# Performance work log

Measured on AMD Instinct MI355X. Metric: run time of the kernel, lower is better.

Reference implementation:

```python
import jax, jax.numpy as jnp
import numpy as np
from math import sqrt

KEY_DIM = 128
N_NODES = 1_000_000
N_GRAPHS = 8192


def setup_inputs() -> dict:
    key = jax.random.key(0)
    k1, k2, k3 = jax.random.split(key, 3)
    V = jax.random.normal(k1, (N_NODES, KEY_DIM), dtype=jnp.float32)
    Q = jax.random.normal(k2, (N_GRAPHS, KEY_DIM), dtype=jnp.float32)
    batch_node_index = jnp.sort(
        jax.random.randint(k3, (N_NODES,), 0, N_GRAPHS, dtype=jnp.int64)
    )
    return {
        "V": V,
        "Q": Q,
        "batch_node_index": batch_node_index,
        "num_graphs": N_GRAPHS,
    }


def reference(V, Q, batch_node_index, num_graphs):
    # scores[v] = <Q[g(v)], V[v]> / sqrt(d)   for each node v in graph g(v)
    scale = jnp.asarray(1.0 / sqrt(KEY_DIM), dtype=V.dtype)
    scores = jnp.einsum("nd,nd->n", Q[batch_node_index], V) * scale  # [N]
    # segment-wise (per-graph) stable softmax
    seg_max = jax.ops.segment_max(scores, batch_node_index, num_segments=num_graphs)
    e = jnp.exp(scores - seg_max[batch_node_index])  # [N]
    denom = jax.ops.segment_sum(e, batch_node_index, num_segments=num_graphs)
    alpha = e / denom[batch_node_index]  # [N]
    # weighted segment sum of node features -> one vector per graph
    H = jax.ops.segment_sum(alpha[:, None] * V, batch_node_index, num_segments=num_graphs)
    return H  # [b, d]
```

## Files before the change

kernel.cpp:

```cpp
#include <hip/hip_runtime.h>

#define KEY_DIM 128
#define GROUPS  8
#define RPG     8
#define CHUNK   (GROUPS*RPG)
#define SCALE   0.08838834764831845f

__device__ __forceinline__ int lower_bound(const int* __restrict__ idx, int n, int key) {
    int lo = 0, hi = n;
    while (lo < hi) {
        int mid = (lo + hi) >> 1;
        if (idx[mid] < key) lo = mid + 1; else hi = mid;
    }
    return lo;
}

__global__ __launch_bounds__(256) void seg_attn_kernel(
        const float* __restrict__ V, const float* __restrict__ Q,
        const int* __restrict__ idx, float* __restrict__ out, int n_nodes) {
    __shared__ float s_max[4];
    __shared__ float s_sum[4];
    __shared__ float s_h[GROUPS * KEY_DIM];

    const int g   = blockIdx.x;
    const int tid = threadIdx.x;
    const int ng  = tid >> 5;
    const int q   = tid & 31;

    const int start = lower_bound(idx, n_nodes, g);
    const int end   = lower_bound(idx, n_nodes, g + 1);

    const float4  q4  = reinterpret_cast<const float4*>(Q)[g * 32 + q];
    const float4* Vf4 = reinterpret_cast<const float4*>(V);

    float4 acc = make_float4(0.f, 0.f, 0.f, 0.f);
    float  m   = -INFINITY;
    float  l   = 0.f;

    for (int cbase = start; cbase < end; cbase += CHUNK) {
        float4 vr[RPG];
        #pragma unroll
        for (int j = 0; j < RPG; ++j) {
            const int i = cbase + ng + j * GROUPS;
            vr[j] = (i < end) ? Vf4[(size_t)i * 32 + q]
                              : make_float4(0.f, 0.f, 0.f, 0.f);
        }

        float p[RPG];
        float lmax = -INFINITY;
        #pragma unroll
        for (int j = 0; j < RPG; ++j) {
            float pp = vr[j].x * q4.x + vr[j].y * q4.y + vr[j].z * q4.z + vr[j].w * q4.w;
            #pragma unroll
            for (int off = 16; off; off >>= 1) pp += __shfl_xor(pp, off);
            const int i = cbase + ng + j * GROUPS;
            p[j] = (i < end) ? pp * SCALE : -INFINITY;
            lmax = fmaxf(lmax, p[j]);
        }

        lmax = fmaxf(lmax, __shfl_xor(lmax, 32));
        if ((tid & 63) == 0) s_max[tid >> 6] = lmax;
        __syncthreads();
        const float cmax = fmaxf(fmaxf(s_max[0], s_max[1]), fmaxf(s_max[2], s_max[3]));

        const float m_new = fmaxf(m, cmax);
        const float r = __expf(m - m_new);
        acc.x *= r; acc.y *= r; acc.z *= r; acc.w *= r;
        l *= r;

        float gsum = 0.f;
        #pragma unroll
        for (int j = 0; j < RPG; ++j) {
            const float e = __expf(p[j] - m_new);
            gsum += e;
            acc.x += e * vr[j].x; acc.y += e * vr[j].y;
            acc.z += e * vr[j].z; acc.w += e * vr[j].w;
        }
        gsum += __shfl_xor(gsum, 32);
        if ((tid & 63) == 0) s_sum[tid >> 6] = gsum;
        __syncthreads();
        l += s_sum[0] + s_sum[1] + s_sum[2] + s_sum[3];
        m = m_new;
    }

    s_h[ng * KEY_DIM + q * 4 + 0] = acc.x;
    s_h[ng * KEY_DIM + q * 4 + 1] = acc.y;
    s_h[ng * KEY_DIM + q * 4 + 2] = acc.z;
    s_h[ng * KEY_DIM + q * 4 + 3] = acc.w;
    __syncthreads();
    if (tid < KEY_DIM) {
        float h = 0.f;
        #pragma unroll
        for (int k = 0; k < GROUPS; ++k) h += s_h[k * KEY_DIM + tid];
        out[(size_t)g * KEY_DIM + tid] = (l > 0.f) ? h / l : 0.f;
    }
}

extern "C" void kernel_launch(void* const* d_in, const int* in_sizes, int n_in,
                              void* d_out, int out_size, void* d_ws, size_t ws_size,
                              hipStream_t stream) {
    const float* V   = (const float*)d_in[0];
    const float* Q   = (const float*)d_in[1];
    const int*   idx = (const int*)d_in[2];
    float*       out = (float*)d_out;

    const int n_nodes    = in_sizes[0] / KEY_DIM;
    const int num_graphs = out_size / KEY_DIM;

    seg_attn_kernel<<<num_graphs, 256, 0, stream>>>(V, Q, idx, out, n_nodes);
}
```

Measured before the change: 102.0 us.

## Precompute segment starts, double-buffer V chunk loads, defer softmax denominator reduction

A separate kernel now writes segment start offsets into the workspace, replacing the per-block binary searches over the index array. The main loop double-buffers V chunk loads in registers so the next chunk's loads are issued before the current chunk is computed, and clamps indices instead of branching on the load. Each thread keeps its own running denominator and reduces it once at the end, which removes one __syncthreads per chunk. The cost is an extra kernel launch, more register use from the second buffer, and a dependency on workspace memory being provided.

```diff
diff --git a/kernel.cpp b/kernel.cpp
--- a/kernel.cpp
+++ b/kernel.cpp
@@ -6,19 +6,21 @@
 #define CHUNK   (GROUPS*RPG)
 #define SCALE   0.08838834764831845f
 
-__device__ __forceinline__ int lower_bound(const int* __restrict__ idx, int n, int key) {
-    int lo = 0, hi = n;
-    while (lo < hi) {
-        int mid = (lo + hi) >> 1;
-        if (idx[mid] < key) lo = mid + 1; else hi = mid;
-    }
-    return lo;
+__global__ __launch_bounds__(256) void seg_starts_kernel(
+        const int* __restrict__ idx, int n, int num_graphs, int* __restrict__ starts) {
+    const int i = blockIdx.x * blockDim.x + threadIdx.x;
+    if (i >= n) return;
+    const int cur  = idx[i];
+    const int prev = (i == 0) ? -1 : idx[i - 1];
+    for (int g = prev + 1; g <= cur; ++g) starts[g] = i;
+    if (i == n - 1)
+        for (int g = cur + 1; g <= num_graphs; ++g) starts[g] = n;
 }
 
 __global__ __launch_bounds__(256) void seg_attn_kernel(
         const float* __restrict__ V, const float* __restrict__ Q,
-        const int* __restrict__ idx, float* __restrict__ out, int n_nodes) {
-    __shared__ float s_max[4];
+        const int* __restrict__ starts, float* __restrict__ out) {
+    __shared__ float s_max[2][4];
     __shared__ float s_sum[4];
     __shared__ float s_h[GROUPS * KEY_DIM];
 
@@ -27,8 +29,8 @@
     const int ng  = tid >> 5;
     const int q   = tid & 31;
 
-    const int start = lower_bound(idx, n_nodes, g);
-    const int end   = lower_bound(idx, n_nodes, g + 1);
+    const int start = starts[g];
+    const int end   = starts[g + 1];
 
     const float4  q4  = reinterpret_cast<const float4*>(Q)[g * 32 + q];
     const float4* Vf4 = reinterpret_cast<const float4*>(V);
@@ -37,62 +39,76 @@
     float  m   = -INFINITY;
     float  l   = 0.f;
 
-    for (int cbase = start; cbase < end; cbase += CHUNK) {
-        float4 vr[RPG];
+    const int nchunks = (end - start + CHUNK - 1) / CHUNK;
+
+    auto load_chunk = [&](float4 (&dst)[RPG], int cbase) {
         #pragma unroll
         for (int j = 0; j < RPG; ++j) {
-            const int i = cbase + ng + j * GROUPS;
-            vr[j] = (i < end) ? Vf4[(size_t)i * 32 + q]
-                              : make_float4(0.f, 0.f, 0.f, 0.f);
+            int i = cbase + ng + j * GROUPS;
+            i = min(i, end - 1);
+            dst[j] = Vf4[(size_t)i * 32 + q];
         }
+    };
 
+    auto compute_chunk = [&](float4 (&buf)[RPG], int c) {
+        const int cbase = start + c * CHUNK;
         float p[RPG];
         float lmax = -INFINITY;
         #pragma unroll
         for (int j = 0; j < RPG; ++j) {
-            float pp = vr[j].x * q4.x + vr[j].y * q4.y + vr[j].z * q4.z + vr[j].w * q4.w;
+            float pp = buf[j].x * q4.x + buf[j].y * q4.y + buf[j].z * q4.z + buf[j].w * q4.w;
             #pragma unroll
             for (int off = 16; off; off >>= 1) pp += __shfl_xor(pp, off);
             const int i = cbase + ng + j * GROUPS;
             p[j] = (i < end) ? pp * SCALE : -INFINITY;
             lmax = fmaxf(lmax, p[j]);
         }
-
         lmax = fmaxf(lmax, __shfl_xor(lmax, 32));
-        if ((tid & 63) == 0) s_max[tid >> 6] = lmax;
+        if ((tid & 63) == 0) s_max[c & 1][tid >> 6] = lmax;
         __syncthreads();
-        const float cmax = fmaxf(fmaxf(s_max[0], s_max[1]), fmaxf(s_max[2], s_max[3]));
-
+        const float cmax = fmaxf(fmaxf(s_max[c & 1][0], s_max[c & 1][1]),
+                                 fmaxf(s_max[c & 1][2], s_max[c & 1][3]));
         const float m_new = fmaxf(m, cmax);
         const float r = __expf(m - m_new);
         acc.x *= r; acc.y *= r; acc.z *= r; acc.w *= r;
         l *= r;
-
-        float gsum = 0.f;
         #pragma unroll
         for (int j = 0; j < RPG; ++j) {
             const float e = __expf(p[j] - m_new);
-            gsum += e;
-            acc.x += e * vr[j].x; acc.y += e * vr[j].y;
-            acc.z += e * vr[j].z; acc.w += e * vr[j].w;
+            l += e;
+            acc.x += e * buf[j].x; acc.y += e * buf[j].y;
+            acc.z += e * buf[j].z; acc.w += e * buf[j].w;
         }
-        gsum += __shfl_xor(gsum, 32);
-        if ((tid & 63) == 0) s_sum[tid >> 6] = gsum;
-        __syncthreads();
-        l += s_sum[0] + s_sum[1] + s_sum[2] + s_sum[3];
         m = m_new;
+    };
+
+    if (nchunks > 0) {
+        float4 vrA[RPG], vrB[RPG];
+        load_chunk(vrA, start);
+        int c = 0;
+        while (true) {
+            if (c + 1 < nchunks) load_chunk(vrB, start + (c + 1) * CHUNK);
+            compute_chunk(vrA, c);
+            if (++c >= nchunks) break;
+            if (c + 1 < nchunks) load_chunk(vrA, start + (c + 1) * CHUNK);
+            compute_chunk(vrB, c);
+            if (++c >= nchunks) break;
+        }
     }
 
+    const float lw = l + __shfl_xor(l, 32);
+    if ((tid & 63) == 0) s_sum[tid >> 6] = lw;
     s_h[ng * KEY_DIM + q * 4 + 0] = acc.x;
     s_h[ng * KEY_DIM + q * 4 + 1] = acc.y;
     s_h[ng * KEY_DIM + q * 4 + 2] = acc.z;
     s_h[ng * KEY_DIM + q * 4 + 3] = acc.w;
     __syncthreads();
     if (tid < KEY_DIM) {
+        const float L = s_sum[0] + s_sum[1] + s_sum[2] + s_sum[3];
         float h = 0.f;
         #pragma unroll
         for (int k = 0; k < GROUPS; ++k) h += s_h[k * KEY_DIM + tid];
-        out[(size_t)g * KEY_DIM + tid] = (l > 0.f) ? h / l : 0.f;
+        out[(size_t)g * KEY_DIM + tid] = (L > 0.f) ? h / L : 0.f;
     }
 }
 
@@ -103,9 +119,11 @@
     const float* Q   = (const float*)d_in[1];
     const int*   idx = (const int*)d_in[2];
     float*       out = (float*)d_out;
+    int*         starts = (int*)d_ws;
 
     const int n_nodes    = in_sizes[0] / KEY_DIM;
     const int num_graphs = out_size / KEY_DIM;
 
-    seg_attn_kernel<<<num_graphs, 256, 0, stream>>>(V, Q, idx, out, n_nodes);
+    seg_starts_kernel<<<(n_nodes + 255) / 256, 256, 0, stream>>>(idx, n_nodes, num_graphs, starts);
+    seg_attn_kernel<<<num_graphs, 256, 0, stream>>>(V, Q, starts, out);
 }
```

New measurement: 98.67 us. -3.3%, faster.
